# Performance work log

Hardware: AMD Instinct MI355X
Metric: run time of the kernel (lower is better)

## Reference

```python
import jax, jax.numpy as jnp
import numpy as np

B, S, D, H = 2, 2048, 1024, 16
HD = D // H

def setup_inputs() -> dict:
    key = jax.random.key(0)
    ks = jax.random.split(key, 9)
    s = 1.0 / np.sqrt(D)
    inp = {"x": jax.random.normal(ks[0], (B, S, D), dtype=jnp.float32)}
    for i, name in enumerate(["q", "k", "v", "g"]):
        inp[f"W{name}"] = jax.random.uniform(ks[1 + i], (D, D), minval=-s, maxval=s, dtype=jnp.float32)
        inp[f"b{name}"] = jax.random.uniform(ks[5 + i], (D,), minval=-s, maxval=s, dtype=jnp.float32)
    return inp

def reference(x, Wq, bq, Wk, bk, Wv, bv, Wg, bg):
    # projections: [B,S,D] -> [B,H,S,HD]
    def proj(W, b):
        y = x @ W.T + b
        return y.reshape(B, S, H, HD).transpose(0, 2, 1, 3)
    q = proj(Wq, bq)
    k = proj(Wk, bk)
    v = proj(Wv, bv)
    g = proj(Wg, bg)
    qg = jax.nn.gelu(q * g, approximate=False)  # gate + activation before scores
    att = jnp.einsum("bhqd,bhkd->bhqk", qg, k)  # note: no 1/sqrt(d) scaling in original
    att = jax.nn.softmax(att, axis=-1)
    out = jnp.einsum("bhqk,bhkd->bhqd", att, v)
    return out.transpose(0, 2, 1, 3).reshape(B, S, D)
```

## Files before the change

### kernel.cpp

```cpp
#include <hip/hip_runtime.h>
#include <hip/hip_bf16.h>
#include <stdint.h>

#define PB 2
#define PS 2048
#define PD 1024
#define PH 16
#define PHD 64
#define PM (PB*PS)

typedef _Float16 half8 __attribute__((ext_vector_type(8)));
typedef _Float16 half4v __attribute__((ext_vector_type(4)));
typedef __fp16   fp16x2 __attribute__((ext_vector_type(2)));
typedef float    f32x4 __attribute__((ext_vector_type(4)));

__device__ __forceinline__ void ld_g2l_16(const void* g, void* l) {
  __builtin_amdgcn_global_load_lds(
      (const __attribute__((address_space(1))) unsigned int*)g,
      (__attribute__((address_space(3))) unsigned int*)l, 16, 0, 0);
}

__global__ void convert_all(const float* __restrict__ x,
                            const float* __restrict__ w0, const float* __restrict__ w1,
                            const float* __restrict__ w2, const float* __restrict__ w3,
                            _Float16* __restrict__ xh, _Float16* __restrict__ wh) {
  int i = blockIdx.x * blockDim.x + threadIdx.x;
  const float* src;
  _Float16* dst;
  int idx;
  if (blockIdx.y == 0) {
    src = x; dst = xh; idx = i;
  } else {
    int wsel = i >> 17;
    idx = i & 131071;
    src = (wsel==0)?w0:(wsel==1)?w1:(wsel==2)?w2:w3;
    dst = wh + (size_t)wsel * 1048576;
  }
  float4 f0 = reinterpret_cast<const float4*>(src)[2*idx];
  float4 f1 = reinterpret_cast<const float4*>(src)[2*idx+1];
  half8 o;
  o[0]=(_Float16)f0.x; o[1]=(_Float16)f0.y; o[2]=(_Float16)f0.z; o[3]=(_Float16)f0.w;
  o[4]=(_Float16)f1.x; o[5]=(_Float16)f1.y; o[6]=(_Float16)f1.z; o[7]=(_Float16)f1.w;
  reinterpret_cast<half8*>(dst)[idx] = o;
}

__global__ __launch_bounds__(256, 3) void proj_gemm(
    const _Float16* __restrict__ xh, const _Float16* __restrict__ wh,
    const float* __restrict__ bqp, const float* __restrict__ bgp,
    const float* __restrict__ bkp, const float* __restrict__ bvp,
    _Float16* __restrict__ qf, _Float16* __restrict__ gf,
    _Float16* __restrict__ kf, _Float16* __restrict__ vT)
{
  const int K = 1024;
  __shared__ _Float16 Sm[16384];
  const int z = blockIdx.z;
  const int wslot = (z==0)?0:(z==1)?3:(z==2)?1:2;
  const size_t woff = (size_t)wslot * (1024*1024);
  const float* bias = (z==0)?bqp:(z==1)?bgp:(z==2)?bkp:bvp;
  _Float16* outp = (z==0)?qf:(z==1)?gf:kf;
  const int m0 = blockIdx.x * 128;
  const int n0 = blockIdx.y * 128;
  const int t = threadIdx.x;
  const int lane = t & 63;
  const int w = t >> 6;
  const int wr = w >> 1, wc = w & 1;
  const int lm = lane & 15, quad = lane >> 4;
  const int scb = (((lane&3) ^ ((lane>>3)&3)))*8;
  const int rblk = ((quad ^ ((lm>>1)&3)))*8;

  auto stage = [&](int buf, int k0) {
    #pragma unroll
    for (int c=0;c<2;c++) {
      int lin = c*256 + t;
      int row = lin >> 2;
      size_t ga = (size_t)(m0+row)*K + k0 + scb;
      size_t gb = (size_t)(n0+row)*K + k0 + scb;
      int lo8 = (c*256 + w*64)*8;
      ld_g2l_16(&xh[ga],        &Sm[buf*4096 + lo8]);
      ld_g2l_16(&wh[woff + gb], &Sm[8192 + buf*4096 + lo8]);
    }
  };

  f32x4 acc[4][4];
  #pragma unroll
  for (int i=0;i<4;i++)
    #pragma unroll
    for (int j=0;j<4;j++) acc[i][j] = (f32x4){0.f,0.f,0.f,0.f};

  stage(0, 0);
  __syncthreads();

  for (int k0 = 0; k0 < K; k0 += 32) {
    const int cur = (k0 >> 5) & 1;
    if (k0 + 32 < K) stage(cur ^ 1, k0 + 32);

    half8 ah[4];
    #pragma unroll
    for (int i=0;i<4;i++)
      ah[i] = *reinterpret_cast<const half8*>(&Sm[cur*4096 + (wr*64 + i*16 + lm)*32 + rblk]);
    #pragma unroll
    for (int j=0;j<4;j++) {
      half8 b = *reinterpret_cast<const half8*>(&Sm[8192 + cur*4096 + (wc*64 + j*16 + lm)*32 + rblk]);
      #pragma unroll
      for (int i=0;i<4;i++)
        acc[i][j] = __builtin_amdgcn_mfma_f32_16x16x32_f16(ah[i], b, acc[i][j], 0,0,0);
    }
    __syncthreads();
  }

  if (z < 3) {
    #pragma unroll
    for (int j=0;j<4;j++) {
      int n = n0 + wc*64 + j*16 + lm;
      float bn = bias[n];
      #pragma unroll
      for (int i=0;i<4;i++) {
        int mb = m0 + wr*64 + i*16 + quad*4;
        #pragma unroll
        for (int r=0;r<4;r++)
          outp[(size_t)(mb+r)*PD + n] = (_Float16)(acc[i][j][r] + bn);
      }
    }
  } else {
    #pragma unroll
    for (int j=0;j<4;j++) {
      int nl = wc*64 + j*16 + lm;
      float bn = bias[n0 + nl];
      #pragma unroll
      for (int i=0;i<4;i++) {
        int tb = wr*64 + i*16 + quad*4;
        half4v pv;
        #pragma unroll
        for (int r=0;r<4;r++) pv[r] = (_Float16)(acc[i][j][r] + bn);
        int sw = (tb >> 3) ^ (nl & 15);
        *reinterpret_cast<half4v*>(&Sm[nl*128 + sw*8 + (tb & 7)]) = pv;
      }
    }
    __syncthreads();
    const int nl2 = t >> 1, co = (t & 1) * 8;
    const int hh = (n0 + nl2) >> 6, dd = (n0 + nl2) & 63;
    const int bb2 = m0 >> 11;
    const size_t vbase = ((size_t)((bb2*16 + hh)*64 + dd))*2048 + (m0 & 2047);
    #pragma unroll
    for (int c=0;c<8;c++) {
      int cc = co + c;
      half8 vv = *reinterpret_cast<const half8*>(&Sm[nl2*128 + ((cc ^ (nl2&15))<<3)]);
      *reinterpret_cast<half8*>(&vT[vbase + cc*8]) = vv;
    }
  }
}

__global__ __launch_bounds__(512) void flash_attn(
    const _Float16* __restrict__ Qf,
    const _Float16* __restrict__ Gf,
    const _Float16* __restrict__ Kp,
    const _Float16* __restrict__ VT,
    float* __restrict__ out)
{
  __shared__ _Float16 Ks[2][64*64];
  __shared__ _Float16 Vts[64*64];
  __shared__ _Float16 Pss[8][16*72];
  const int t = threadIdx.x;
  const int lane = t & 63, w = t >> 6;
  const int lm = lane & 15, quad = lane >> 4;
  const int bh = blockIdx.y;
  const int b = bh >> 4, h = bh & 15;
  const int qb = blockIdx.x * 128 + w * 16;
  const size_t kbase = (size_t)b * PS * PD + (size_t)h * PHD;
  const size_t vtb = (size_t)bh * 64 * 2048;

  const int lrow = lane >> 3;
  const int lcb  = ((lane & 7) ^ lrow) * 8;
  const int kblk0 = ((quad     ^ (lm&7)))*8;
  const int kblk1 = (((quad+4) ^ (lm&7)))*8;

  half8 qgf[2];
  {
    size_t qrow = kbase + (size_t)(qb + lm) * PD;
    half8 q0 = *reinterpret_cast<const half8*>(&Qf[qrow + quad*8]);
    half8 q1 = *reinterpret_cast<const half8*>(&Qf[qrow + 32 + quad*8]);
    half8 g0 = *reinterpret_cast<const half8*>(&Gf[qrow + quad*8]);
    half8 g1 = *reinterpret_cast<const half8*>(&Gf[qrow + 32 + quad*8]);
    #pragma unroll
    for (int e=0;e<8;e++) {
      float x0 = (float)q0[e] * (float)g0[e];
      float x1 = (float)q1[e] * (float)g1[e];
      float y0 = 0.5f * x0 * (1.0f + erff(x0 * 0.70710678118f));
      float y1 = 0.5f * x1 * (1.0f + erff(x1 * 0.70710678118f));
      qgf[0][e] = (_Float16)(y0 * 1.44269504f);
      qgf[1][e] = (_Float16)(y1 * 1.44269504f);
    }
  }

  half8 ones;
  #pragma unroll
  for (int e=0;e<8;e++) ones[e] = (_Float16)1.0f;

  f32x4 o[4];
  #pragma unroll
  for (int dc=0;dc<4;dc++) o[dc] = (f32x4){0.f,0.f,0.f,0.f};
  f32x4 o4 = (f32x4){0.f,0.f,0.f,0.f};

  const _Float16* kgp = &Kp[kbase + (size_t)(w*8 + lrow)*PD + lcb];
  const _Float16* vgp = &VT[vtb + (size_t)(w*8 + lrow)*2048 + lcb];
  _Float16* vdst0 = &Vts[((w*8 + lrow)*8 + (lane & 7))*8];

  const f32x4 sinit = {-11.54156036f, -11.54156036f, -11.54156036f, -11.54156036f};

  ld_g2l_16(kgp, &Ks[0][(w*8)*64]);
  ld_g2l_16(vgp, &Vts[(w*8)*64]);
  __syncthreads();

  for (int kt = 0; kt < PS; kt += 64) {
    const int buf = (kt >> 6) & 1;
    const bool nx = (kt + 64) < PS;
    float4 vr0;
    if (nx) {
      ld_g2l_16(kgp + (size_t)(kt+64)*PD, &Ks[buf^1][(w*8)*64]);
      vr0 = *reinterpret_cast<const float4*>(vgp + kt + 64);
    }

    f32x4 s[4];
    __builtin_amdgcn_s_setprio(1);
    #pragma unroll
    for (int ns=0; ns<4; ns++) {
      const int rb = (ns*16 + lm)*64;
      half8 kf0 = *reinterpret_cast<const half8*>(&Ks[buf][rb + kblk0]);
      half8 kf1 = *reinterpret_cast<const half8*>(&Ks[buf][rb + kblk1]);
      f32x4 a = sinit;
      a = __builtin_amdgcn_mfma_f32_16x16x32_f16(kf0, qgf[0], a, 0,0,0);
      a = __builtin_amdgcn_mfma_f32_16x16x32_f16(kf1, qgf[1], a, 0,0,0);
      s[ns] = a;
    }
    __builtin_amdgcn_s_setprio(0);

    #pragma unroll
    for (int ns=0; ns<4; ns++) {
      float p0 = fminf(__builtin_amdgcn_exp2f(s[ns][0]), 60000.0f);
      float p1 = fminf(__builtin_amdgcn_exp2f(s[ns][1]), 60000.0f);
      float p2 = fminf(__builtin_amdgcn_exp2f(s[ns][2]), 60000.0f);
      float p3 = fminf(__builtin_amdgcn_exp2f(s[ns][3]), 60000.0f);
      union { struct { fp16x2 a, b; } s2; half4v v; } u;
      u.s2.a = __builtin_amdgcn_cvt_pkrtz(p0, p1);
      u.s2.b = __builtin_amdgcn_cvt_pkrtz(p2, p3);
      *reinterpret_cast<half4v*>(&Pss[w][lm*72 + ns*16 + quad*4]) = u.v;
    }

    half8 pa0 = *reinterpret_cast<const half8*>(&Pss[w][lm*72 + quad*8]);
    half8 pa1 = *reinterpret_cast<const half8*>(&Pss[w][lm*72 + 32 + quad*8]);
    __builtin_amdgcn_s_setprio(1);
    #pragma unroll
    for (int dc=0;dc<4;dc++) {
      const int vb = (dc*16 + lm)*64;
      half8 vb0 = *reinterpret_cast<const half8*>(&Vts[vb + kblk0]);
      half8 vb1 = *reinterpret_cast<const half8*>(&Vts[vb + kblk1]);
      o[dc] = __builtin_amdgcn_mfma_f32_16x16x32_f16(pa0, vb0, o[dc], 0,0,0);
      o[dc] = __builtin_amdgcn_mfma_f32_16x16x32_f16(pa1, vb1, o[dc], 0,0,0);
    }
    o4 = __builtin_amdgcn_mfma_f32_16x16x32_f16(pa0, ones, o4, 0,0,0);
    o4 = __builtin_amdgcn_mfma_f32_16x16x32_f16(pa1, ones, o4, 0,0,0);
    __builtin_amdgcn_s_setprio(0);

    __syncthreads();
    if (nx) {
      *reinterpret_cast<float4*>(vdst0) = vr0;
    }
    __syncthreads();
  }

  #pragma unroll
  for (int r=0;r<4;r++) {
    float invr = 1.0f / o4[r];
    int row = qb + quad*4 + r;
    size_t ob = kbase + (size_t)row * PD;
    #pragma unroll
    for (int dc=0;dc<4;dc++) {
      out[ob + dc*16 + lm] = o[dc][r] * invr;
    }
  }
}

extern "C" void kernel_launch(void* const* d_in, const int* in_sizes, int n_in,
                              void* d_out, int out_size, void* d_ws, size_t ws_size,
                              hipStream_t stream) {
  const float* x  = (const float*)d_in[0];
  const float* Wq = (const float*)d_in[1];
  const float* bq = (const float*)d_in[2];
  const float* Wk = (const float*)d_in[3];
  const float* bk = (const float*)d_in[4];
  const float* Wv = (const float*)d_in[5];
  const float* bv = (const float*)d_in[6];
  const float* Wg = (const float*)d_in[7];
  const float* bg = (const float*)d_in[8];
  float* out = (float*)d_out;

  char* ws = (char*)d_ws;
  const size_t MB = 1u << 20;
  _Float16* xh = (_Float16*)(ws + 0*MB);
  _Float16* wh = (_Float16*)(ws + 8*MB);
  _Float16* qf = (_Float16*)(ws + 16*MB);
  _Float16* gf = (_Float16*)(ws + 24*MB);
  _Float16* kf = (_Float16*)(ws + 32*MB);
  _Float16* vT = (_Float16*)(ws + 40*MB);

  convert_all<<<dim3(2048, 2), 256, 0, stream>>>(x, Wq, Wk, Wv, Wg, xh, wh);

  proj_gemm<<<dim3(PM/128, PD/128, 4), 256, 0, stream>>>(
      xh, wh, bq, bg, bk, bv, qf, gf, kf, vT);

  flash_attn<<<dim3(PS/128, PB*PH), 512, 0, stream>>>(qf, gf, kf, vT, out);
}
```

Measured before the change: 183.7 us.

## Give each attention wave two 16-row query tiles, halving waves per block

The flash attention block shrinks from 8 waves to 4, and each wave now handles 32 query rows as two 16-row MFMA tiles. Each K and V fragment read from LDS is reused for both tiles, which halves LDS reads per MFMA. Exp and pack now run inline after each score MFMA instead of in a separate loop. The cost is twice the accumulator and Q-fragment registers per wave, fewer waves to hide latency, and each thread issuing two K/V loads per tile.

Result: slower. 187.5 us (+2.0%).

```diff
diff --git a/kernel.cpp b/kernel.cpp
--- a/kernel.cpp
+++ b/kernel.cpp
@@ -150,7 +150,7 @@
   }
 }
 
-__global__ __launch_bounds__(512) void flash_attn(
+__global__ __launch_bounds__(256, 2) void flash_attn(
     const _Float16* __restrict__ Qf,
     const _Float16* __restrict__ Gf,
     const _Float16* __restrict__ Kp,
@@ -159,13 +159,13 @@
 {
   __shared__ _Float16 Ks[2][64*64];
   __shared__ _Float16 Vts[64*64];
-  __shared__ _Float16 Pss[8][16*72];
+  __shared__ _Float16 Pss[4][32*72];
   const int t = threadIdx.x;
   const int lane = t & 63, w = t >> 6;
   const int lm = lane & 15, quad = lane >> 4;
   const int bh = blockIdx.y;
   const int b = bh >> 4, h = bh & 15;
-  const int qb = blockIdx.x * 128 + w * 16;
+  const int qb = blockIdx.x * 128 + w * 32;
   const size_t kbase = (size_t)b * PS * PD + (size_t)h * PHD;
   const size_t vtb = (size_t)bh * 64 * 2048;
 
@@ -174,9 +174,10 @@
   const int kblk0 = ((quad     ^ (lm&7)))*8;
   const int kblk1 = (((quad+4) ^ (lm&7)))*8;
 
-  half8 qgf[2];
-  {
-    size_t qrow = kbase + (size_t)(qb + lm) * PD;
+  half8 qgf[2][2];
+  #pragma unroll
+  for (int mm=0; mm<2; mm++) {
+    size_t qrow = kbase + (size_t)(qb + mm*16 + lm) * PD;
     half8 q0 = *reinterpret_cast<const half8*>(&Qf[qrow + quad*8]);
     half8 q1 = *reinterpret_cast<const half8*>(&Qf[qrow + 32 + quad*8]);
     half8 g0 = *reinterpret_cast<const half8*>(&Gf[qrow + quad*8]);
@@ -187,8 +188,8 @@
       float x1 = (float)q1[e] * (float)g1[e];
       float y0 = 0.5f * x0 * (1.0f + erff(x0 * 0.70710678118f));
       float y1 = 0.5f * x1 * (1.0f + erff(x1 * 0.70710678118f));
-      qgf[0][e] = (_Float16)(y0 * 1.44269504f);
-      qgf[1][e] = (_Float16)(y1 * 1.44269504f);
+      qgf[mm][0][e] = (_Float16)(y0 * 1.44269504f);
+      qgf[mm][1][e] = (_Float16)(y1 * 1.44269504f);
     }
   }
 
@@ -196,86 +197,106 @@
   #pragma unroll
   for (int e=0;e<8;e++) ones[e] = (_Float16)1.0f;
 
-  f32x4 o[4];
-  #pragma unroll
-  for (int dc=0;dc<4;dc++) o[dc] = (f32x4){0.f,0.f,0.f,0.f};
-  f32x4 o4 = (f32x4){0.f,0.f,0.f,0.f};
+  f32x4 o[2][4];
+  #pragma unroll
+  for (int mm=0;mm<2;mm++)
+    #pragma unroll
+    for (int dc=0;dc<4;dc++) o[mm][dc] = (f32x4){0.f,0.f,0.f,0.f};
+  f32x4 o4[2];
+  o4[0] = (f32x4){0.f,0.f,0.f,0.f};
+  o4[1] = (f32x4){0.f,0.f,0.f,0.f};
 
   const _Float16* kgp = &Kp[kbase + (size_t)(w*8 + lrow)*PD + lcb];
   const _Float16* vgp = &VT[vtb + (size_t)(w*8 + lrow)*2048 + lcb];
   _Float16* vdst0 = &Vts[((w*8 + lrow)*8 + (lane & 7))*8];
+  _Float16* vdst1 = vdst0 + 32*64;
 
   const f32x4 sinit = {-11.54156036f, -11.54156036f, -11.54156036f, -11.54156036f};
 
-  ld_g2l_16(kgp, &Ks[0][(w*8)*64]);
-  ld_g2l_16(vgp, &Vts[(w*8)*64]);
+  ld_g2l_16(kgp,                   &Ks[0][(w*8)*64]);
+  ld_g2l_16(kgp + (size_t)32*PD,   &Ks[0][(32 + w*8)*64]);
+  ld_g2l_16(vgp,                   &Vts[(w*8)*64]);
+  ld_g2l_16(vgp + (size_t)32*2048, &Vts[(32 + w*8)*64]);
   __syncthreads();
 
   for (int kt = 0; kt < PS; kt += 64) {
     const int buf = (kt >> 6) & 1;
     const bool nx = (kt + 64) < PS;
-    float4 vr0;
+    float4 vr0, vr1;
     if (nx) {
       ld_g2l_16(kgp + (size_t)(kt+64)*PD, &Ks[buf^1][(w*8)*64]);
+      ld_g2l_16(kgp + (size_t)(kt+96)*PD, &Ks[buf^1][(32 + w*8)*64]);
       vr0 = *reinterpret_cast<const float4*>(vgp + kt + 64);
-    }
-
-    f32x4 s[4];
+      vr1 = *reinterpret_cast<const float4*>(vgp + (size_t)32*2048 + kt + 64);
+    }
+
     __builtin_amdgcn_s_setprio(1);
     #pragma unroll
     for (int ns=0; ns<4; ns++) {
       const int rb = (ns*16 + lm)*64;
       half8 kf0 = *reinterpret_cast<const half8*>(&Ks[buf][rb + kblk0]);
       half8 kf1 = *reinterpret_cast<const half8*>(&Ks[buf][rb + kblk1]);
-      f32x4 a = sinit;
-      a = __builtin_amdgcn_mfma_f32_16x16x32_f16(kf0, qgf[0], a, 0,0,0);
-      a = __builtin_amdgcn_mfma_f32_16x16x32_f16(kf1, qgf[1], a, 0,0,0);
-      s[ns] = a;
+      #pragma unroll
+      for (int mm=0; mm<2; mm++) {
+        f32x4 a = sinit;
+        a = __builtin_amdgcn_mfma_f32_16x16x32_f16(kf0, qgf[mm][0], a, 0,0,0);
+        a = __builtin_amdgcn_mfma_f32_16x16x32_f16(kf1, qgf[mm][1], a, 0,0,0);
+        float p0 = fminf(__builtin_amdgcn_exp2f(a[0]), 60000.0f);
+        float p1 = fminf(__builtin_amdgcn_exp2f(a[1]), 60000.0f);
+        float p2 = fminf(__builtin_amdgcn_exp2f(a[2]), 60000.0f);
+        float p3 = fminf(__builtin_amdgcn_exp2f(a[3]), 60000.0f);
+        union { struct { fp16x2 a, b; } s2; half4v v; } u;
+        u.s2.a = __builtin_amdgcn_cvt_pkrtz(p0, p1);
+        u.s2.b = __builtin_amdgcn_cvt_pkrtz(p2, p3);
+        *reinterpret_cast<half4v*>(&Pss[w][(mm*16 + lm)*72 + ns*16 + quad*4]) = u.v;
+      }
     }
     __builtin_amdgcn_s_setprio(0);
 
-    #pragma unroll
-    for (int ns=0; ns<4; ns++) {
-      float p0 = fminf(__builtin_amdgcn_exp2f(s[ns][0]), 60000.0f);
-      float p1 = fminf(__builtin_amdgcn_exp2f(s[ns][1]), 60000.0f);
-      float p2 = fminf(__builtin_amdgcn_exp2f(s[ns][2]), 60000.0f);
-      float p3 = fminf(__builtin_amdgcn_exp2f(s[ns][3]), 60000.0f);
-      union { struct { fp16x2 a, b; } s2; half4v v; } u;
-      u.s2.a = __builtin_amdgcn_cvt_pkrtz(p0, p1);
-      u.s2.b = __builtin_amdgcn_cvt_pkrtz(p2, p3);
-      *reinterpret_cast<half4v*>(&Pss[w][lm*72 + ns*16 + quad*4]) = u.v;
-    }
-
-    half8 pa0 = *reinterpret_cast<const half8*>(&Pss[w][lm*72 + quad*8]);
-    half8 pa1 = *reinterpret_cast<const half8*>(&Pss[w][lm*72 + 32 + quad*8]);
+    half8 pa0[2], pa1[2];
+    #pragma unroll
+    for (int mm=0; mm<2; mm++) {
+      pa0[mm] = *reinterpret_cast<const half8*>(&Pss[w][(mm*16 + lm)*72 + quad*8]);
+      pa1[mm] = *reinterpret_cast<const half8*>(&Pss[w][(mm*16 + lm)*72 + 32 + quad*8]);
+    }
     __builtin_amdgcn_s_setprio(1);
     #pragma unroll
     for (int dc=0;dc<4;dc++) {
       const int vb = (dc*16 + lm)*64;
       half8 vb0 = *reinterpret_cast<const half8*>(&Vts[vb + kblk0]);
       half8 vb1 = *reinterpret_cast<const half8*>(&Vts[vb + kblk1]);
-      o[dc] = __builtin_amdgcn_mfma_f32_16x16x32_f16(pa0, vb0, o[dc], 0,0,0);
-      o[dc] = __builtin_amdgcn_mfma_f32_16x16x32_f16(pa1, vb1, o[dc], 0,0,0);
-    }
-    o4 = __builtin_amdgcn_mfma_f32_16x16x32_f16(pa0, ones, o4, 0,0,0);
-    o4 = __builtin_amdgcn_mfma_f32_16x16x32_f16(pa1, ones, o4, 0,0,0);
+      #pragma unroll
+      for (int mm=0; mm<2; mm++) {
+        o[mm][dc] = __builtin_amdgcn_mfma_f32_16x16x32_f16(pa0[mm], vb0, o[mm][dc], 0,0,0);
+        o[mm][dc] = __builtin_amdgcn_mfma_f32_16x16x32_f16(pa1[mm], vb1, o[mm][dc], 0,0,0);
+      }
+    }
+    #pragma unroll
+    for (int mm=0; mm<2; mm++) {
+      o4[mm] = __builtin_amdgcn_mfma_f32_16x16x32_f16(pa0[mm], ones, o4[mm], 0,0,0);
+      o4[mm] = __builtin_amdgcn_mfma_f32_16x16x32_f16(pa1[mm], ones, o4[mm], 0,0,0);
+    }
     __builtin_amdgcn_s_setprio(0);
 
     __syncthreads();
     if (nx) {
       *reinterpret_cast<float4*>(vdst0) = vr0;
+      *reinterpret_cast<float4*>(vdst1) = vr1;
     }
     __syncthreads();
   }
 
   #pragma unroll
-  for (int r=0;r<4;r++) {
-    float invr = 1.0f / o4[r];
-    int row = qb + quad*4 + r;
-    size_t ob = kbase + (size_t)row * PD;
-    #pragma unroll
-    for (int dc=0;dc<4;dc++) {
-      out[ob + dc*16 + lm] = o[dc][r] * invr;
+  for (int mm=0; mm<2; mm++) {
+    #pragma unroll
+    for (int r=0;r<4;r++) {
+      float invr = 1.0f / o4[mm][r];
+      int row = qb + mm*16 + quad*4 + r;
+      size_t ob = kbase + (size_t)row * PD;
+      #pragma unroll
+      for (int dc=0;dc<4;dc++) {
+        out[ob + dc*16 + lm] = o[mm][dc][r] * invr;
+      }
     }
   }
 }
@@ -308,5 +329,5 @@
   proj_gemm<<<dim3(PM/128, PD/128, 4), 256, 0, stream>>>(
       xh, wh, bq, bg, bk, bv, qf, gf, kf, vT);
 
-  flash_attn<<<dim3(PS/128, PB*PH), 512, 0, stream>>>(qf, gf, kf, vT, out);
-}
+  flash_attn<<<dim3(PS/128, PB*PH), 256, 0, stream>>>(qf, gf, kf, vT, out);
+}
```
